# Optimization experiments

Hardware: AMD Instinct MI355X
Metric: run time of the kernel (lower is better)

Reference implementation:

```python
import jax, jax.numpy as jnp
import numpy as np

B, L, S = 128, 80, 8          # dialogues, utterances per dialogue, speakers
NODE_DIM, HIDDEN, HEADS, OUT_DIM = 768, 512, 8, 256
N = B * L


def _build_edges():
    """Replicates InterSentenceGNN.build_graph + Batch.from_data_list offsets."""
    rel = np.zeros((N, 3), np.float32)
    all_e, last = [], []
    eye3 = np.eye(3, dtype=np.float32)
    for b in range(B):
        off = b * L
        u = L - 1
        e, t = [], []
        for i in range(L):
            if i > 0:
                e += [[i - 1, i], [i, i - 1]]; t += [0, 0]   # REL_SEQ
            if i < u:
                e += [[i, u], [u, i]]; t += [1, 1]           # REL_CTX
        for s in range(S):                                   # REL_SPK, round-robin speakers
            g = list(range(s, L, S))
            for a in range(len(g)):
                for c in range(a + 1, len(g)):
                    e += [[g[a], g[c]], [g[c], g[a]]]; t += [2, 2]
        e = np.asarray(e, np.int64); t = np.asarray(t, np.int64)
        np.add.at(rel, e[:, 0] + off, eye3[t])               # out-degree per relation (pre-unique)
        all_e.append(np.unique(e, axis=0) + off)             # torch.unique(idx, dim=1)
        last.append(off + u)
    edge_index = np.concatenate(all_e, 0).T.astype(np.int32)  # [2, E], row0=src, row1=dst
    return edge_index, rel, np.asarray(last, np.int32)


def setup_inputs() -> dict:
    key = jax.random.key(0)
    ks = jax.random.split(key, 16)
    edge_index, rel_feat, last_idx = _build_edges()
    g = lambda k, shp, fan: jax.random.normal(k, shp, jnp.float32) * (1.0 / np.sqrt(fan))
    return {
        "x": jax.random.normal(ks[0], (N, NODE_DIM), jnp.float32),
        "rel_feat": jnp.asarray(rel_feat),
        "w1": g(ks[1], (3, 64), 3), "b1": jnp.zeros((64,), jnp.float32),
        "w2": g(ks[2], (64, 1), 64), "b2": jnp.zeros((1,), jnp.float32),
        "Wl1": g(ks[3], (NODE_DIM, HIDDEN), NODE_DIM), "bl1": jnp.zeros((HIDDEN,), jnp.float32),
        "Wr1": g(ks[4], (NODE_DIM, HIDDEN), NODE_DIM), "br1": jnp.zeros((HIDDEN,), jnp.float32),
        "att1": g(ks[5], (HEADS, HIDDEN // HEADS), HIDDEN // HEADS),
        "bias1": jnp.zeros((HIDDEN,), jnp.float32),
        "Wl2": g(ks[6], (HIDDEN, OUT_DIM), HIDDEN), "bl2": jnp.zeros((OUT_DIM,), jnp.float32),
        "Wr2": g(ks[7], (HIDDEN, OUT_DIM), HIDDEN), "br2": jnp.zeros((OUT_DIM,), jnp.float32),
        "att2": g(ks[8], (1, OUT_DIM), OUT_DIM),
        "bias2": jnp.zeros((OUT_DIM,), jnp.float32),
        "ln_g": jnp.ones((OUT_DIM,), jnp.float32), "ln_b": jnp.zeros((OUT_DIM,), jnp.float32),
        "edge_index": jnp.asarray(edge_index),
        "last_idx": jnp.asarray(last_idx),
    }


def _gatv2(x, Wl, bl, Wr, br, att, bias, src, dst, heads, ch, concat):
    """PyG GATv2Conv (eval mode, self-loops already in src/dst)."""
    n = x.shape[0]
    xl = (x @ Wl + bl).reshape(n, heads, ch)   # source transform (messages)
    xr = (x @ Wr + br).reshape(n, heads, ch)   # target transform
    e = jax.nn.leaky_relu(xl[src] + xr[dst], negative_slope=0.2)  # [E,H,C]
    logit = jnp.einsum("ehc,hc->eh", e, att)                      # [E,H]
    m = jax.ops.segment_max(logit, dst, num_segments=n)
    a = jnp.exp(logit - m[dst])
    denom = jax.ops.segment_sum(a, dst, num_segments=n)
    alpha = a / denom[dst]                                        # segment softmax over dst
    msg = (xl[src] * alpha[:, :, None]).reshape(-1, heads * ch)
    out = jax.ops.segment_sum(msg, dst, num_segments=n).reshape(n, heads, ch)
    out = out.reshape(n, heads * ch) if concat else out.mean(axis=1)
    return out + bias


def reference(x, rel_feat, w1, b1, w2, b2, Wl1, bl1, Wr1, br1, att1, bias1,
              Wl2, bl2, Wr2, br2, att2, bias2, ln_g, ln_b, edge_index, last_idx):
    n = x.shape[0]
    loops = jnp.arange(n, dtype=edge_index.dtype)
    src = jnp.concatenate([edge_index[0], loops])  # add_self_loops=True (PyG default)
    dst = jnp.concatenate([edge_index[1], loops])
    w = jax.nn.sigmoid(jax.nn.relu(rel_feat @ w1 + b1) @ w2 + b2)  # [N,1] node gate
    h = x * w
    h = jax.nn.elu(_gatv2(h, Wl1, bl1, Wr1, br1, att1, bias1, src, dst, HEADS, HIDDEN // HEADS, True))
    h = _gatv2(h, Wl2, bl2, Wr2, br2, att2, bias2, src, dst, 1, OUT_DIM, False)
    mu = jnp.mean(h, axis=-1, keepdims=True)
    var = jnp.mean((h - mu) ** 2, axis=-1, keepdims=True)
    h = (h - mu) * jax.lax.rsqrt(var + 1e-5) * ln_g + ln_b
    return h[last_idx]  # x[batch.ptr[1:] - 1]: last (context) node per dialogue
```

## Files before the change

kernel.cpp:

```cpp
#include <hip/hip_runtime.h>
#include <hip/hip_bf16.h>

#define NN 10240
#define LL 80
#define BB 128

typedef _Float16 half8 __attribute__((ext_vector_type(8)));
typedef _Float16 half2v __attribute__((ext_vector_type(2)));
typedef float f32x4 __attribute__((ext_vector_type(4)));

#define GLD16(gptr, lptr)                                                        \
  __builtin_amdgcn_global_load_lds(                                              \
      (const __attribute__((address_space(1))) void*)(gptr),                     \
      (__attribute__((address_space(3))) void*)(lptr), 16, 0, 0)

__device__ __forceinline__ float dot2f(half2v a, half2v b, float c) {
#if __has_builtin(__builtin_amdgcn_fdot2)
  return __builtin_amdgcn_fdot2(a, b, c, false);
#else
  return c + (float)a.x * (float)b.x + (float)a.y * (float)b.y;
#endif
}
__device__ __forceinline__ half2v u2h(unsigned int u) { half2v r; __builtin_memcpy(&r, &u, 4); return r; }
__device__ __forceinline__ unsigned int h2u(half2v h) { unsigned int u; __builtin_memcpy(&u, &h, 4); return u; }
__device__ __forceinline__ int roff(int r) { return r * 72; }

__device__ __forceinline__ float dotq4r(uint4 a, uint4 b, const half2v* atv, int qb, float acc) {
  const half2v c02 = {(_Float16)0.2f, (_Float16)0.2f};
  unsigned int aa[4] = {a.x, a.y, a.z, a.w};
  unsigned int bb[4] = {b.x, b.y, b.z, b.w};
#pragma unroll
  for (int j = 0; j < 4; ++j) {
    half2v e = u2h(aa[j]) + u2h(bb[j]);
    half2v l = __builtin_elementwise_max(e, e * c02);
    acc = dot2f(l, atv[qb + j], acc);
  }
  return acc;
}

__global__ __launch_bounds__(256) void prep_all(
    const float* __restrict__ x, const float* __restrict__ rel,
    const float* __restrict__ w1, const float* __restrict__ b1,
    const float* __restrict__ w2, const float* __restrict__ b2,
    const float* __restrict__ Wl1, const float* __restrict__ Wr1,
    const float* __restrict__ Wl2, const float* __restrict__ Wr2,
    const float* __restrict__ bl1, const float* __restrict__ br1,
    const float* __restrict__ att1,
    _Float16* __restrict__ h0, _Float16* __restrict__ Wt1,
    _Float16* __restrict__ Wt2cat,
    float* __restrict__ biasc, _Float16* __restrict__ att_h) {
  __shared__ float tile[32][33];
  int bid = blockIdx.x;
  int tid = threadIdx.x;
  if (bid < 2560) {
    int wave = tid >> 6, l = tid & 63;
    int n = bid * 4 + wave;
    float r0 = rel[n * 3 + 0], r1 = rel[n * 3 + 1], r2 = rel[n * 3 + 2];
    float v = r0 * w1[l] + r1 * w1[64 + l] + r2 * w1[128 + l] + b1[l];
    v = v > 0.f ? v : 0.f;
    v *= w2[l];
    for (int d = 32; d; d >>= 1) v += __shfl_down(v, d, 64);
    float s = __shfl(v, 0, 64);
    float g = 1.f / (1.f + __expf(-(s + b2[0])));
    const float4* xr = (const float4*)(x + (size_t)n * 768);
    _Float16* hr = h0 + (size_t)n * 768;
#pragma unroll
    for (int i = 0; i < 3; ++i) {
      int f = i * 64 + l;
      float4 xv = xr[f];
      half2v p0 = {(_Float16)(xv.x * g), (_Float16)(xv.y * g)};
      half2v p1 = {(_Float16)(xv.z * g), (_Float16)(xv.w * g)};
      uint2 ov = {h2u(p0), h2u(p1)};
      *(uint2*)&hr[f * 4] = ov;
    }
    return;
  }
  int r = bid - 2560;
  const float* W;
  _Float16* Wt;
  int K, Nc, bx, by;
  if (r < 384)      { W = Wl1; Wt = Wt1;                          K = 768; Nc = 512; bx = r % 16;       by = r / 16; }
  else if (r < 768) { W = Wr1; Wt = Wt1 + (size_t)512 * 768;      K = 768; Nc = 512; bx = (r-384) % 16; by = (r-384) / 16; }
  else if (r < 896) { W = Wl2; Wt = Wt2cat;                       K = 512; Nc = 256; bx = (r-768) % 8;  by = (r-768) / 8; }
  else if (r < 1024){ W = Wr2; Wt = Wt2cat + (size_t)256 * 512;   K = 512; Nc = 256; bx = (r-896) % 8;  by = (r-896) / 8; }
  else {
    for (int i = tid; i < 1024; i += 256) biasc[i] = (i < 512) ? bl1[i] : br1[i - 512];
    for (int i = tid; i < 512; i += 256) att_h[i] = (_Float16)att1[i];
    return;
  }
  int n0 = bx * 32, k0 = by * 32;
  int c = tid & 31, rr = tid >> 5;
#pragma unroll
  for (int p = 0; p < 4; ++p) {
    int rw = p * 8 + rr;
    tile[rw][c] = W[(size_t)(k0 + rw) * Nc + n0 + c];
  }
  __syncthreads();
#pragma unroll
  for (int p = 0; p < 4; ++p) {
    int rw = p * 8 + rr;
    Wt[(size_t)(n0 + rw) * K + k0 + c] = (_Float16)tile[c][rw];
  }
}

__global__ __launch_bounds__(512, 6) void gemm1gat1(
    const _Float16* __restrict__ h0, const _Float16* __restrict__ Wt1,
    const float* __restrict__ biasc, const _Float16* __restrict__ att_h,
    const float* __restrict__ bias1, _Float16* __restrict__ h1) {
  __shared__ __align__(16) char smem[53248];
  _Float16* Ab = (_Float16*)smem;
  _Float16* Bb = (_Float16*)(smem + 20480);
  _Float16* s_xl = (_Float16*)smem;
  _Float16* s_xr = (_Float16*)(smem + 11520);
  float* s_logit = (float*)(smem + 23040);
  signed char* s_src8 = (signed char*)(smem + 27200);
  float* s_hub = (float*)(smem + 28240);
  _Float16* s_xlT = (_Float16*)(smem + 28560);
  _Float16* s_P = (_Float16*)smem;

  int bx = blockIdx.x;
  int h = bx >> 7, b = bx & 127;
  int base = b * LL;
  int tid = threadIdx.x;
  int wave = tid >> 6, lane = tid & 63;
  int lr = lane & 15, lk = lane >> 4;

  int segA8 = ((lane & 7) ^ ((lane >> 3) & 7)) * 8;
  int r0a = wave * 16 + (lane >> 3);
  const _Float16* aP0 = h0;
  const _Float16* aP1 = h0;
  if (wave < 5) {
    aP0 = h0 + (size_t)(base + r0a) * 768 + segA8;
    aP1 = h0 + (size_t)(base + r0a + 8) * 768 + segA8;
  }
  int rb0 = r0a, rb1 = r0a + 8;
  int wr0 = (rb0 < 64) ? (h * 64 + rb0) : (512 + h * 64 + (rb0 - 64));
  int wr1 = (rb1 < 64) ? (h * 64 + rb1) : (512 + h * 64 + (rb1 - 64));
  const _Float16* bP0 = Wt1 + (size_t)wr0 * 768 + segA8;
  const _Float16* bP1 = Wt1 + (size_t)wr1 * 768 + segA8;

  f32x4 acc[5] = {};
  if (wave < 5) {
    GLD16(aP0, Ab + wave * 1024);
    GLD16(aP1, Ab + wave * 1024 + 512);
  }
  GLD16(bP0, Bb + wave * 1024);
  GLD16(bP1, Bb + wave * 1024 + 512);
  __syncthreads();
  for (int t = 0; t < 12; ++t) {
    int cur = t & 1;
    if (t < 11) {
      int k0 = (t + 1) * 64;
      int nb = cur ^ 1;
      if (wave < 5) {
        GLD16(aP0 + k0, Ab + nb * 5120 + wave * 1024);
        GLD16(aP1 + k0, Ab + nb * 5120 + wave * 1024 + 512);
      }
      GLD16(bP0 + k0, Bb + nb * 8192 + wave * 1024);
      GLD16(bP1 + k0, Bb + nb * 8192 + wave * 1024 + 512);
    }
    const _Float16* Ac = Ab + cur * 5120;
    const _Float16* Bc = Bb + cur * 8192;
    int rB = wave * 16 + lr;
#pragma unroll
    for (int s2 = 0; s2 < 2; ++s2) {
      int cx = ((s2 * 4 + lk) ^ (lr & 7)) * 8;
      half8 bf = *(const half8*)(Bc + rB * 64 + cx);
#pragma unroll
      for (int m = 0; m < 5; ++m) {
        half8 af = *(const half8*)(Ac + (m * 16 + lr) * 64 + cx);
        acc[m] = __builtin_amdgcn_mfma_f32_16x16x32_f16(af, bf, acc[m], 0, 0, 0);
      }
    }
    __syncthreads();
  }
  {
    int c = wave * 16 + lr;
    bool isxl = c < 64;
    int cc = isxl ? c : c - 64;
    float bb = biasc[(isxl ? 0 : 512) + h * 64 + cc];
    _Float16* dst = isxl ? s_xl : s_xr;
#pragma unroll
    for (int m = 0; m < 5; ++m)
#pragma unroll
      for (int rg = 0; rg < 4; ++rg) {
        int row = m * 16 + lk * 4 + rg;
        _Float16 hv = (_Float16)(acc[m][rg] + bb);
        dst[roff(row) + cc] = hv;
        if (isxl) s_xlT[cc * 88 + row] = hv;
      }
  }
  if (tid < 79) {
    int d = tid;
    signed char list[13];
    int c = 0;
    list[c++] = (signed char)d;
    if (d > 0) list[c++] = (signed char)(d - 1);
    if (d + 1 < 79) list[c++] = (signed char)(d + 1);
    list[c++] = 79;
    for (int j = d & 7; j < 80; j += 8)
      if (j != d && j != 79) list[c++] = (signed char)j;
    for (int i = c; i < 13; ++i) list[i] = -1;
#pragma unroll
    for (int i = 0; i < 13; ++i) s_src8[i * 80 + d] = list[i];
  }
  __syncthreads();

  const unsigned int* pat = (const unsigned int*)(att_h + h * 64);
  half2v atv[32];
#pragma unroll
  for (int q = 0; q < 32; ++q) atv[q] = u2h(__builtin_amdgcn_readfirstlane(pat[q]));
  if (tid < 474) {
    int d = tid / 6, io = tid % 6;
    const uint4* pxr = (const uint4*)(s_xr + roff(d));
    uint4 xrr[8];
#pragma unroll
    for (int q = 0; q < 8; ++q) xrr[q] = pxr[q];
#pragma unroll
    for (int k = 0; k < 3; ++k) {
      int i = io + 6 * k;
      if (i < 13) {
        int src = s_src8[i * 80 + d];
        if (src < 0) {
          s_logit[i * 80 + d] = -3e38f;
        } else {
          const uint4* pxl = (const uint4*)(s_xl + roff(src));
          float a2 = 0.f;
#pragma unroll
          for (int q = 0; q < 8; ++q) a2 = dotq4r(pxl[q], xrr[q], atv, q * 4, a2);
          s_logit[i * 80 + d] = a2;
        }
      }
    }
  } else {
    int j = tid - 474;
    const uint4* pxr = (const uint4*)(s_xr + roff(79));
    uint4 xrr[8];
#pragma unroll
    for (int q = 0; q < 8; ++q) xrr[q] = pxr[q];
#pragma unroll
    for (int k = 0; k < 3; ++k) {
      int s = j + 38 * k;
      if (s < 80) {
        const uint4* pxl = (const uint4*)(s_xl + roff(s));
        float a2 = 0.f;
#pragma unroll
        for (int q = 0; q < 8; ++q) a2 = dotq4r(pxl[q], xrr[q], atv, q * 4, a2);
        s_hub[s] = a2;
      }
    }
  }
  __syncthreads();

  {
    uint4 z4 = {0u, 0u, 0u, 0u};
    for (int z = tid; z < 1040; z += 512) ((uint4*)smem)[z] = z4;
  }
  float va[13], inv_d = 0.f;
  bool isd = tid < 79;
  if (isd) {
    int d = tid;
    float m = -3e38f;
#pragma unroll
    for (int i = 0; i < 13; ++i) { va[i] = s_logit[i * 80 + d]; m = fmaxf(m, va[i]); }
    float sum = 0.f;
#pragma unroll
    for (int i = 0; i < 13; ++i) { va[i] = __expf(va[i] - m); sum += va[i]; }
    inv_d = 1.f / sum;
  }
  float he0 = 0.f, he1 = 0.f, hinv = 0.f;
  if (wave == 7) {
    int l = lane;
    float v0 = s_hub[l];
    float v1 = (l < 16) ? s_hub[64 + l] : -3e38f;
    float m = fmaxf(v0, v1);
    for (int d = 32; d; d >>= 1) m = fmaxf(m, __shfl_xor(m, d, 64));
    he0 = __expf(v0 - m);
    he1 = (l < 16) ? __expf(v1 - m) : 0.f;
    float sum = he0 + he1;
    for (int d = 32; d; d >>= 1) sum += __shfl_xor(sum, d, 64);
    hinv = 1.f / sum;
  }
  __syncthreads();

  if (isd) {
    int d = tid;
#pragma unroll
    for (int i = 0; i < 13; ++i) {
      int src = s_src8[i * 80 + d];
      if (src >= 0) s_P[d * 104 + src] = (_Float16)(va[i] * inv_d);
    }
  }
  if (wave == 7) {
    int l = lane;
    s_P[79 * 104 + l] = (_Float16)(he0 * hinv);
    if (l < 16) s_P[79 * 104 + 64 + l] = (_Float16)(he1 * hinv);
  }
  __syncthreads();

  {
    int nt = (wave < 4) ? 3 : 2;
    int tb = (wave < 4) ? wave * 3 : 12 + (wave - 4) * 2;
    for (int tt = 0; tt < nt; ++tt) {
      int t = tb + tt;
      int m = t >> 2, n = t & 3;
      f32x4 a = {};
#pragma unroll
      for (int kc = 0; kc < 3; ++kc) {
        half8 af = *(const half8*)(s_P + (m * 16 + lr) * 104 + kc * 32 + lk * 8);
        half8 bf = *(const half8*)(s_xlT + (n * 16 + lr) * 88 + kc * 32 + lk * 8);
        a = __builtin_amdgcn_mfma_f32_16x16x32_f16(af, bf, a, 0, 0, 0);
      }
      int c = n * 16 + lr;
      float bb = bias1[h * 64 + c];
#pragma unroll
      for (int rg = 0; rg < 4; ++rg) {
        int d = m * 16 + lk * 4 + rg;
        float v = a[rg] + bb;
        v = v > 0.f ? v : __expf(v) - 1.f;
        h1[(size_t)(base + d) * 512 + h * 64 + c] = (_Float16)v;
      }
    }
  }
}

__global__ __launch_bounds__(256) void gemm2a(
    const _Float16* __restrict__ h1, const _Float16* __restrict__ Bt,
    const float* __restrict__ bl2, _Float16* __restrict__ xl2) {
  __shared__ __align__(16) char smem[16384];
  _Float16* Ab = (_Float16*)smem;
  _Float16* Bb = (_Float16*)(smem + 8192);
  int bx = blockIdx.x;
  int mb = bx >> 2, nb = bx & 3;
  int tid = threadIdx.x;
  int wave = tid >> 6, lane = tid & 63;
  int lr = lane & 15, lk = lane >> 4;
  int seg8 = ((lane & 3) ^ ((lane >> 3) & 3)) * 8;
  int row = tid >> 2;
  const _Float16* aP = h1 + (size_t)(mb * 64 + row) * 512 + seg8;
  const _Float16* bP = Bt + (size_t)(nb * 64 + row) * 512 + seg8;
  int xk8 = (lk ^ ((lr >> 1) & 3)) * 8;
  f32x4 acc[4] = {};
  GLD16(aP, Ab + wave * 512);
  GLD16(bP, Bb + wave * 512);
  __syncthreads();
  for (int t = 0; t < 16; ++t) {
    int cur = t & 1;
    if (t < 15) {
      int k0 = (t + 1) * 32;
      int nbuf = cur ^ 1;
      GLD16(aP + k0, Ab + nbuf * 2048 + wave * 512);
      GLD16(bP + k0, Bb + nbuf * 2048 + wave * 512);
    }
    const _Float16* Ac = Ab + cur * 2048;
    const _Float16* Bc = Bb + cur * 2048;
    half8 bf = *(const half8*)(Bc + (wave * 16 + lr) * 32 + xk8);
#pragma unroll
    for (int m = 0; m < 4; ++m) {
      half8 af = *(const half8*)(Ac + (m * 16 + lr) * 32 + xk8);
      acc[m] = __builtin_amdgcn_mfma_f32_16x16x32_f16(af, bf, acc[m], 0, 0, 0);
    }
    __syncthreads();
  }
  int col = nb * 64 + wave * 16 + lr;
  float bb = bl2[col];
#pragma unroll
  for (int m = 0; m < 4; ++m)
#pragma unroll
    for (int rg = 0; rg < 4; ++rg) {
      int r = mb * 64 + m * 16 + lk * 4 + rg;
      xl2[(size_t)r * 256 + col] = (_Float16)(acc[m][rg] + bb);
    }
}

#define PX 264
__global__ __launch_bounds__(512) void gat2ln(
    const _Float16* __restrict__ h1, const _Float16* __restrict__ xl2,
    const _Float16* __restrict__ Bt, const float* __restrict__ br2,
    const float* __restrict__ att2, const float* __restrict__ bias2,
    const float* __restrict__ ln_g, const float* __restrict__ ln_b,
    float* __restrict__ out) {
  __shared__ __align__(16) _Float16 s_x[80 * PX];
  __shared__ _Float16 s_att[256];
  __shared__ _Float16 s_xr[256];
  __shared__ float s_red[80];
  __shared__ float s_sum[4], s_sq[4];

  int b = blockIdx.x;
  int tid = threadIdx.x;
  int wave = tid >> 6, lane = tid & 63;

  if (tid < 256) s_att[tid] = (_Float16)att2[tid];
  for (int t = tid; t < 2560; t += 512) {
    int row = t >> 5, q = t & 31;
    uint4 v = *(const uint4*)(xl2 + ((size_t)(b * 80 + row)) * 256 + q * 8);
    *(uint4*)(s_x + row * PX + q * 8) = v;
  }
  {
    int c = tid >> 1, kh = tid & 1;
    const uint4* wr = (const uint4*)(Bt + (size_t)(256 + c) * 512 + kh * 256);
    const uint4* hq = (const uint4*)(h1 + (size_t)(b * 80 + 79) * 512 + kh * 256);
    float s = 0.f;
#pragma unroll 8
    for (int q = 0; q < 32; ++q) {
      uint4 ua = hq[q], uw = wr[q];
      s = dot2f(u2h(ua.x), u2h(uw.x), s);
      s = dot2f(u2h(ua.y), u2h(uw.y), s);
      s = dot2f(u2h(ua.z), u2h(uw.z), s);
      s = dot2f(u2h(ua.w), u2h(uw.w), s);
    }
    s += __shfl_xor(s, 1, 64);
    if (kh == 0) s_xr[c] = (_Float16)(s + br2[c]);
  }
  __syncthreads();
  if (tid < 160) {
    int r = tid >> 1, hf = tid & 1;
    const half2v* xa = (const half2v*)(s_x + r * PX + hf * 128);
    const half2v* xr = (const half2v*)(s_xr + hf * 128);
    const half2v* at = (const half2v*)(s_att + hf * 128);
    float lg = 0.f;
    const half2v c02 = {(_Float16)0.2f, (_Float16)0.2f};
#pragma unroll
    for (int q = 0; q < 64; ++q) {
      half2v e = xa[q] + xr[q];
      half2v l = __builtin_elementwise_max(e, e * c02);
      lg = dot2f(l, at[q], lg);
    }
    lg += __shfl_xor(lg, 1, 64);
    if (hf == 0) s_red[r] = lg;
  }
  __syncthreads();
  if (wave == 7) {
    float v0 = s_red[lane];
    float v1 = (lane < 16) ? s_red[64 + lane] : -3e38f;
    float m = fmaxf(v0, v1);
    for (int d = 32; d; d >>= 1) m = fmaxf(m, __shfl_xor(m, d, 64));
    float e0 = __expf(v0 - m);
    float e1 = (lane < 16) ? __expf(v1 - m) : 0.f;
    float sum = e0 + e1;
    for (int d = 32; d; d >>= 1) sum += __shfl_xor(sum, d, 64);
    float inv = 1.f / sum;
    s_red[lane] = e0 * inv;
    if (lane < 16) s_red[64 + lane] = e1 * inv;
  }
  __syncthreads();
  float v = 0.f;
  if (tid < 256) {
    float a = 0.f;
#pragma unroll
    for (int r = 0; r < 80; ++r) a += s_red[r] * (float)s_x[r * PX + tid];
    v = a + bias2[tid];
    float p = v;
    for (int d = 32; d; d >>= 1) p += __shfl_down(p, d, 64);
    if (lane == 0) s_sum[wave] = p;
    float q = v * v;
    for (int d = 32; d; d >>= 1) q += __shfl_down(q, d, 64);
    if (lane == 0) s_sq[wave] = q;
  }
  __syncthreads();
  if (tid < 256) {
    float mu = (s_sum[0] + s_sum[1] + s_sum[2] + s_sum[3]) * (1.f / 256.f);
    float ex2 = (s_sq[0] + s_sq[1] + s_sq[2] + s_sq[3]) * (1.f / 256.f);
    float var = ex2 - mu * mu;
    float r = rsqrtf(var + 1e-5f);
    out[b * 256 + tid] = (v - mu) * r * ln_g[tid] + ln_b[tid];
  }
}

extern "C" void kernel_launch(void* const* d_in, const int* in_sizes, int n_in,
                              void* d_out, int out_size, void* d_ws, size_t ws_size,
                              hipStream_t stream) {
  const float* x      = (const float*)d_in[0];
  const float* rel    = (const float*)d_in[1];
  const float* w1     = (const float*)d_in[2];
  const float* b1     = (const float*)d_in[3];
  const float* w2     = (const float*)d_in[4];
  const float* b2     = (const float*)d_in[5];
  const float* Wl1    = (const float*)d_in[6];
  const float* bl1    = (const float*)d_in[7];
  const float* Wr1    = (const float*)d_in[8];
  const float* br1    = (const float*)d_in[9];
  const float* att1   = (const float*)d_in[10];
  const float* bias1  = (const float*)d_in[11];
  const float* Wl2    = (const float*)d_in[12];
  const float* bl2    = (const float*)d_in[13];
  const float* Wr2    = (const float*)d_in[14];
  const float* br2    = (const float*)d_in[15];
  const float* att2   = (const float*)d_in[16];
  const float* bias2  = (const float*)d_in[17];
  const float* ln_g   = (const float*)d_in[18];
  const float* ln_b   = (const float*)d_in[19];
  float* out = (float*)d_out;

  char* p = (char*)d_ws;
  _Float16* h0     = (_Float16*)p; p += (size_t)NN * 768 * 2;
  _Float16* h1     = (_Float16*)p; p += (size_t)NN * 512 * 2;
  _Float16* Wt1    = (_Float16*)p; p += (size_t)1024 * 768 * 2;
  _Float16* Wt2cat = (_Float16*)p; p += (size_t)512 * 512 * 2;
  _Float16* att_h  = (_Float16*)p; p += 1024;
  float* biasc     = (float*)p; p += 1024 * 4;
  _Float16* xl2    = (_Float16*)p; p += (size_t)NN * 256 * 2;

  prep_all<<<2560 + 1025, 256, 0, stream>>>(x, rel, w1, b1, w2, b2, Wl1, Wr1, Wl2, Wr2,
                                            bl1, br1, att1, h0, Wt1, Wt2cat, biasc, att_h);

  gemm1gat1<<<1024, 512, 0, stream>>>(h0, Wt1, biasc, att_h, bias1, h1);

  gemm2a<<<640, 256, 0, stream>>>(h1, Wt2cat, bl2, xl2);

  gat2ln<<<BB, 512, 0, stream>>>(h1, xl2, Wt2cat, br2, att2, bias2, ln_g, ln_b, out);
}
```

Measured before the change: 179.8 us.

## Process two attention heads per block in fused GEMM1+GAT1 kernel

Each block of the fused projection plus first-layer attention kernel now computes two heads instead of one, so the grid is halved. The block loads its slab of node features once and multiplies it against both heads' weight columns, using a narrower 32-wide K step with a new swizzle. The attention and softmax stage then runs twice in sequence, once per head, over separate shared-memory buffers. This halves the global reads of the node features and drops the grid to one wave of resident blocks, at the cost of a larger shared-memory footprint (lower occupancy), twice the accumulator registers, and more serialized work per block.

```diff
diff --git a/kernel.cpp b/kernel.cpp
--- a/kernel.cpp
+++ b/kernel.cpp
@@ -107,88 +107,89 @@
     const _Float16* __restrict__ h0, const _Float16* __restrict__ Wt1,
     const float* __restrict__ biasc, const _Float16* __restrict__ att_h,
     const float* __restrict__ bias1, _Float16* __restrict__ h1) {
-  __shared__ __align__(16) char smem[53248];
+  __shared__ __align__(16) char smem[74240];
   _Float16* Ab = (_Float16*)smem;
-  _Float16* Bb = (_Float16*)(smem + 20480);
-  _Float16* s_xl = (_Float16*)smem;
-  _Float16* s_xr = (_Float16*)(smem + 11520);
-  float* s_logit = (float*)(smem + 23040);
-  signed char* s_src8 = (signed char*)(smem + 27200);
-  float* s_hub = (float*)(smem + 28240);
-  _Float16* s_xlT = (_Float16*)(smem + 28560);
+  _Float16* Bb = (_Float16*)(smem + 10240);
+  _Float16* s_xl0 = (_Float16*)smem;
+  _Float16* s_xr0 = (_Float16*)(smem + 11520);
+  _Float16* s_xl1 = (_Float16*)(smem + 23040);
+  _Float16* s_xr1 = (_Float16*)(smem + 34560);
+  float* s_logit = (float*)(smem + 46080);
+  signed char* s_src8 = (signed char*)(smem + 50240);
+  float* s_hub = (float*)(smem + 51280);
+  _Float16* s_xlT0 = (_Float16*)(smem + 51600);
+  _Float16* s_xlT1 = (_Float16*)(smem + 62864);
   _Float16* s_P = (_Float16*)smem;
 
   int bx = blockIdx.x;
-  int h = bx >> 7, b = bx & 127;
+  int hp = bx >> 7, b = bx & 127;
   int base = b * LL;
   int tid = threadIdx.x;
   int wave = tid >> 6, lane = tid & 63;
   int lr = lane & 15, lk = lane >> 4;
 
-  int segA8 = ((lane & 7) ^ ((lane >> 3) & 7)) * 8;
-  int r0a = wave * 16 + (lane >> 3);
-  const _Float16* aP0 = h0;
-  const _Float16* aP1 = h0;
+  int seg8 = ((lane & 3) ^ ((lane >> 3) & 3)) * 8;
+  const _Float16* aP = h0;
   if (wave < 5) {
-    aP0 = h0 + (size_t)(base + r0a) * 768 + segA8;
-    aP1 = h0 + (size_t)(base + r0a + 8) * 768 + segA8;
-  }
-  int rb0 = r0a, rb1 = r0a + 8;
-  int wr0 = (rb0 < 64) ? (h * 64 + rb0) : (512 + h * 64 + (rb0 - 64));
-  int wr1 = (rb1 < 64) ? (h * 64 + rb1) : (512 + h * 64 + (rb1 - 64));
-  const _Float16* bP0 = Wt1 + (size_t)wr0 * 768 + segA8;
-  const _Float16* bP1 = Wt1 + (size_t)wr1 * 768 + segA8;
-
-  f32x4 acc[5] = {};
-  if (wave < 5) {
-    GLD16(aP0, Ab + wave * 1024);
-    GLD16(aP1, Ab + wave * 1024 + 512);
-  }
+    int c = wave * 64 + lane;
+    aP = h0 + (size_t)(base + (c >> 2)) * 768 + seg8;
+  }
+  int c0 = wave * 128 + lane;
+  int r0 = c0 >> 2, r1 = (c0 + 64) >> 2;
+  int rh0 = r0 & 127, rh1 = r1 & 127;
+  int hh0 = hp * 2 + (r0 >> 7), hh1 = hp * 2 + (r1 >> 7);
+  int w0 = (rh0 < 64) ? (hh0 * 64 + rh0) : (512 + hh0 * 64 + (rh0 - 64));
+  int w1 = (rh1 < 64) ? (hh1 * 64 + rh1) : (512 + hh1 * 64 + (rh1 - 64));
+  const _Float16* bP0 = Wt1 + (size_t)w0 * 768 + seg8;
+  const _Float16* bP1 = Wt1 + (size_t)w1 * 768 + seg8;
+  int xk8 = (lk ^ ((lr >> 1) & 3)) * 8;
+
+  f32x4 acc[5][2] = {};
+  if (wave < 5) GLD16(aP, Ab + wave * 512);
   GLD16(bP0, Bb + wave * 1024);
   GLD16(bP1, Bb + wave * 1024 + 512);
   __syncthreads();
-  for (int t = 0; t < 12; ++t) {
+  for (int t = 0; t < 24; ++t) {
     int cur = t & 1;
-    if (t < 11) {
-      int k0 = (t + 1) * 64;
+    if (t < 23) {
+      int k0 = (t + 1) * 32;
       int nb = cur ^ 1;
-      if (wave < 5) {
-        GLD16(aP0 + k0, Ab + nb * 5120 + wave * 1024);
-        GLD16(aP1 + k0, Ab + nb * 5120 + wave * 1024 + 512);
-      }
+      if (wave < 5) GLD16(aP + k0, Ab + nb * 2560 + wave * 512);
       GLD16(bP0 + k0, Bb + nb * 8192 + wave * 1024);
       GLD16(bP1 + k0, Bb + nb * 8192 + wave * 1024 + 512);
     }
-    const _Float16* Ac = Ab + cur * 5120;
+    const _Float16* Ac = Ab + cur * 2560;
     const _Float16* Bc = Bb + cur * 8192;
-    int rB = wave * 16 + lr;
-#pragma unroll
-    for (int s2 = 0; s2 < 2; ++s2) {
-      int cx = ((s2 * 4 + lk) ^ (lr & 7)) * 8;
-      half8 bf = *(const half8*)(Bc + rB * 64 + cx);
-#pragma unroll
-      for (int m = 0; m < 5; ++m) {
-        half8 af = *(const half8*)(Ac + (m * 16 + lr) * 64 + cx);
-        acc[m] = __builtin_amdgcn_mfma_f32_16x16x32_f16(af, bf, acc[m], 0, 0, 0);
-      }
+    half8 bf0 = *(const half8*)(Bc + (wave * 16 + lr) * 32 + xk8);
+    half8 bf1 = *(const half8*)(Bc + ((wave + 8) * 16 + lr) * 32 + xk8);
+#pragma unroll
+    for (int m = 0; m < 5; ++m) {
+      half8 af = *(const half8*)(Ac + (m * 16 + lr) * 32 + xk8);
+      acc[m][0] = __builtin_amdgcn_mfma_f32_16x16x32_f16(af, bf0, acc[m][0], 0, 0, 0);
+      acc[m][1] = __builtin_amdgcn_mfma_f32_16x16x32_f16(af, bf1, acc[m][1], 0, 0, 0);
     }
     __syncthreads();
   }
   {
-    int c = wave * 16 + lr;
-    bool isxl = c < 64;
-    int cc = isxl ? c : c - 64;
-    float bb = biasc[(isxl ? 0 : 512) + h * 64 + cc];
-    _Float16* dst = isxl ? s_xl : s_xr;
-#pragma unroll
-    for (int m = 0; m < 5; ++m)
-#pragma unroll
-      for (int rg = 0; rg < 4; ++rg) {
-        int row = m * 16 + lk * 4 + rg;
-        _Float16 hv = (_Float16)(acc[m][rg] + bb);
-        dst[roff(row) + cc] = hv;
-        if (isxl) s_xlT[cc * 88 + row] = hv;
-      }
+    int c2 = wave * 16 + lr;
+    bool isxl = c2 < 64;
+    int cc = isxl ? c2 : c2 - 64;
+#pragma unroll
+    for (int hj = 0; hj < 2; ++hj) {
+      int h = hp * 2 + hj;
+      float bb = biasc[(isxl ? 0 : 512) + h * 64 + cc];
+      _Float16* dst = hj ? (isxl ? s_xl1 : s_xr1) : (isxl ? s_xl0 : s_xr0);
+      _Float16* xlT = hj ? s_xlT1 : s_xlT0;
+#pragma unroll
+      for (int m = 0; m < 5; ++m)
+#pragma unroll
+        for (int rg = 0; rg < 4; ++rg) {
+          int row = m * 16 + lk * 4 + rg;
+          _Float16 hv = (_Float16)(acc[m][hj][rg] + bb);
+          dst[roff(row) + cc] = hv;
+          if (isxl) xlT[cc * 88 + row] = hv;
+        }
+    }
   }
   if (tid < 79) {
     int d = tid;
@@ -206,121 +207,128 @@
   }
   __syncthreads();
 
-  const unsigned int* pat = (const unsigned int*)(att_h + h * 64);
-  half2v atv[32];
-#pragma unroll
-  for (int q = 0; q < 32; ++q) atv[q] = u2h(__builtin_amdgcn_readfirstlane(pat[q]));
-  if (tid < 474) {
-    int d = tid / 6, io = tid % 6;
-    const uint4* pxr = (const uint4*)(s_xr + roff(d));
-    uint4 xrr[8];
-#pragma unroll
-    for (int q = 0; q < 8; ++q) xrr[q] = pxr[q];
-#pragma unroll
-    for (int k = 0; k < 3; ++k) {
-      int i = io + 6 * k;
-      if (i < 13) {
-        int src = s_src8[i * 80 + d];
-        if (src < 0) {
-          s_logit[i * 80 + d] = -3e38f;
-        } else {
-          const uint4* pxl = (const uint4*)(s_xl + roff(src));
-          float a2 = 0.f;
-#pragma unroll
-          for (int q = 0; q < 8; ++q) a2 = dotq4r(pxl[q], xrr[q], atv, q * 4, a2);
-          s_logit[i * 80 + d] = a2;
+  for (int hj = 0; hj < 2; ++hj) {
+    int h = hp * 2 + hj;
+    _Float16* xlC = hj ? s_xl1 : s_xl0;
+    _Float16* xrC = hj ? s_xr1 : s_xr0;
+    _Float16* xlTC = hj ? s_xlT1 : s_xlT0;
+    const unsigned int* pat = (const unsigned int*)(att_h + h * 64);
+    half2v atv[32];
+#pragma unroll
+    for (int q = 0; q < 32; ++q) atv[q] = u2h(__builtin_amdgcn_readfirstlane(pat[q]));
+    if (tid < 474) {
+      int d = tid / 6, io = tid % 6;
+      const uint4* pxr = (const uint4*)(xrC + roff(d));
+      uint4 xrr[8];
+#pragma unroll
+      for (int q = 0; q < 8; ++q) xrr[q] = pxr[q];
+#pragma unroll
+      for (int k = 0; k < 3; ++k) {
+        int i = io + 6 * k;
+        if (i < 13) {
+          int src = s_src8[i * 80 + d];
+          if (src < 0) {
+            s_logit[i * 80 + d] = -3e38f;
+          } else {
+            const uint4* pxl = (const uint4*)(xlC + roff(src));
+            float a2 = 0.f;
+#pragma unroll
+            for (int q = 0; q < 8; ++q) a2 = dotq4r(pxl[q], xrr[q], atv, q * 4, a2);
+            s_logit[i * 80 + d] = a2;
+          }
         }
       }
-    }
-  } else {
-    int j = tid - 474;
-    const uint4* pxr = (const uint4*)(s_xr + roff(79));
-    uint4 xrr[8];
-#pragma unroll
-    for (int q = 0; q < 8; ++q) xrr[q] = pxr[q];
-#pragma unroll
-    for (int k = 0; k < 3; ++k) {
-      int s = j + 38 * k;
-      if (s < 80) {
-        const uint4* pxl = (const uint4*)(s_xl + roff(s));
-        float a2 = 0.f;
-#pragma unroll
-        for (int q = 0; q < 8; ++q) a2 = dotq4r(pxl[q], xrr[q], atv, q * 4, a2);
-        s_hub[s] = a2;
+    } else {
+      int j = tid - 474;
+      const uint4* pxr = (const uint4*)(xrC + roff(79));
+      uint4 xrr[8];
+#pragma unroll
+      for (int q = 0; q < 8; ++q) xrr[q] = pxr[q];
+#pragma unroll
+      for (int k = 0; k < 3; ++k) {
+        int s = j + 38 * k;
+        if (s < 80) {
+          const uint4* pxl = (const uint4*)(xlC + roff(s));
+          float a2 = 0.f;
+#pragma unroll
+          for (int q = 0; q < 8; ++q) a2 = dotq4r(pxl[q], xrr[q], atv, q * 4, a2);
+          s_hub[s] = a2;
+        }
       }
     }
-  }
-  __syncthreads();
-
-  {
-    uint4 z4 = {0u, 0u, 0u, 0u};
-    for (int z = tid; z < 1040; z += 512) ((uint4*)smem)[z] = z4;
-  }
-  float va[13], inv_d = 0.f;
-  bool isd = tid < 79;
-  if (isd) {
-    int d = tid;
-    float m = -3e38f;
-#pragma unroll
-    for (int i = 0; i < 13; ++i) { va[i] = s_logit[i * 80 + d]; m = fmaxf(m, va[i]); }
-    float sum = 0.f;
-#pragma unroll
-    for (int i = 0; i < 13; ++i) { va[i] = __expf(va[i] - m); sum += va[i]; }
-    inv_d = 1.f / sum;
-  }
-  float he0 = 0.f, he1 = 0.f, hinv = 0.f;
-  if (wave == 7) {
-    int l = lane;
-    float v0 = s_hub[l];
-    float v1 = (l < 16) ? s_hub[64 + l] : -3e38f;
-    float m = fmaxf(v0, v1);
-    for (int d = 32; d; d >>= 1) m = fmaxf(m, __shfl_xor(m, d, 64));
-    he0 = __expf(v0 - m);
-    he1 = (l < 16) ? __expf(v1 - m) : 0.f;
-    float sum = he0 + he1;
-    for (int d = 32; d; d >>= 1) sum += __shfl_xor(sum, d, 64);
-    hinv = 1.f / sum;
-  }
-  __syncthreads();
-
-  if (isd) {
-    int d = tid;
-#pragma unroll
-    for (int i = 0; i < 13; ++i) {
-      int src = s_src8[i * 80 + d];
-      if (src >= 0) s_P[d * 104 + src] = (_Float16)(va[i] * inv_d);
-    }
-  }
-  if (wave == 7) {
-    int l = lane;
-    s_P[79 * 104 + l] = (_Float16)(he0 * hinv);
-    if (l < 16) s_P[79 * 104 + 64 + l] = (_Float16)(he1 * hinv);
-  }
-  __syncthreads();
-
-  {
-    int nt = (wave < 4) ? 3 : 2;
-    int tb = (wave < 4) ? wave * 3 : 12 + (wave - 4) * 2;
-    for (int tt = 0; tt < nt; ++tt) {
-      int t = tb + tt;
-      int m = t >> 2, n = t & 3;
-      f32x4 a = {};
-#pragma unroll
-      for (int kc = 0; kc < 3; ++kc) {
-        half8 af = *(const half8*)(s_P + (m * 16 + lr) * 104 + kc * 32 + lk * 8);
-        half8 bf = *(const half8*)(s_xlT + (n * 16 + lr) * 88 + kc * 32 + lk * 8);
-        a = __builtin_amdgcn_mfma_f32_16x16x32_f16(af, bf, a, 0, 0, 0);
+    __syncthreads();
+
+    {
+      uint4 z4 = {0u, 0u, 0u, 0u};
+      for (int z = tid; z < 1040; z += 512) ((uint4*)smem)[z] = z4;
+    }
+    float va[13], inv_d = 0.f;
+    bool isd = tid < 79;
+    if (isd) {
+      int d = tid;
+      float m = -3e38f;
+#pragma unroll
+      for (int i = 0; i < 13; ++i) { va[i] = s_logit[i * 80 + d]; m = fmaxf(m, va[i]); }
+      float sum = 0.f;
+#pragma unroll
+      for (int i = 0; i < 13; ++i) { va[i] = __expf(va[i] - m); sum += va[i]; }
+      inv_d = 1.f / sum;
+    }
+    float he0 = 0.f, he1 = 0.f, hinv = 0.f;
+    if (wave == 7) {
+      int l = lane;
+      float v0 = s_hub[l];
+      float v1 = (l < 16) ? s_hub[64 + l] : -3e38f;
+      float m = fmaxf(v0, v1);
+      for (int d = 32; d; d >>= 1) m = fmaxf(m, __shfl_xor(m, d, 64));
+      he0 = __expf(v0 - m);
+      he1 = (l < 16) ? __expf(v1 - m) : 0.f;
+      float sum = he0 + he1;
+      for (int d = 32; d; d >>= 1) sum += __shfl_xor(sum, d, 64);
+      hinv = 1.f / sum;
+    }
+    __syncthreads();
+
+    if (isd) {
+      int d = tid;
+#pragma unroll
+      for (int i = 0; i < 13; ++i) {
+        int src = s_src8[i * 80 + d];
+        if (src >= 0) s_P[d * 104 + src] = (_Float16)(va[i] * inv_d);
       }
-      int c = n * 16 + lr;
-      float bb = bias1[h * 64 + c];
-#pragma unroll
-      for (int rg = 0; rg < 4; ++rg) {
-        int d = m * 16 + lk * 4 + rg;
-        float v = a[rg] + bb;
-        v = v > 0.f ? v : __expf(v) - 1.f;
-        h1[(size_t)(base + d) * 512 + h * 64 + c] = (_Float16)v;
+    }
+    if (wave == 7) {
+      int l = lane;
+      s_P[79 * 104 + l] = (_Float16)(he0 * hinv);
+      if (l < 16) s_P[79 * 104 + 64 + l] = (_Float16)(he1 * hinv);
+    }
+    __syncthreads();
+
+    {
+      int nt = (wave < 4) ? 3 : 2;
+      int tb = (wave < 4) ? wave * 3 : 12 + (wave - 4) * 2;
+      for (int tt = 0; tt < nt; ++tt) {
+        int t = tb + tt;
+        int m = t >> 2, n = t & 3;
+        f32x4 a = {};
+#pragma unroll
+        for (int kc = 0; kc < 3; ++kc) {
+          half8 af = *(const half8*)(s_P + (m * 16 + lr) * 104 + kc * 32 + lk * 8);
+          half8 bf = *(const half8*)(xlTC + (n * 16 + lr) * 88 + kc * 32 + lk * 8);
+          a = __builtin_amdgcn_mfma_f32_16x16x32_f16(af, bf, a, 0, 0, 0);
+        }
+        int c = n * 16 + lr;
+        float bb = bias1[h * 64 + c];
+#pragma unroll
+        for (int rg = 0; rg < 4; ++rg) {
+          int d = m * 16 + lk * 4 + rg;
+          float v = a[rg] + bb;
+          v = v > 0.f ? v : __expf(v) - 1.f;
+          h1[(size_t)(base + d) * 512 + h * 64 + c] = (_Float16)v;
+        }
       }
     }
+    __syncthreads();
   }
 }
 
@@ -504,7 +512,7 @@
   prep_all<<<2560 + 1025, 256, 0, stream>>>(x, rel, w1, b1, w2, b2, Wl1, Wr1, Wl2, Wr2,
                                             bl1, br1, att1, h0, Wt1, Wt2cat, biasc, att_h);
 
-  gemm1gat1<<<1024, 512, 0, stream>>>(h0, Wt1, biasc, att_h, bias1, h1);
+  gemm1gat1<<<512, 512, 0, stream>>>(h0, Wt1, biasc, att_h, bias1, h1);
 
   gemm2a<<<640, 256, 0, stream>>>(h1, Wt2cat, bl2, xl2);
 
```

After: 182.0 us. No clear change (+1.3%).

## Halve GEMM1 K-tile to 32 to cut LDS and raise occupancy

Applied to the files above, without the earlier changes.

The fused GEMM+GAT layer-1 kernel now stages 32-wide K tiles instead of 64-wide ones. Each lane issues one global-to-LDS load per operand per step, with a new XOR swizzle, and the loop runs 24 steps instead of 12. This shrinks the shared-memory footprint so launch bounds can request 8 blocks per SM instead of 6, trading more barriers and loop iterations for higher occupancy. It also adds explicit zeroing of the padding region of the transposed xl buffer.

```diff
diff --git a/kernel.cpp b/kernel.cpp
--- a/kernel.cpp
+++ b/kernel.cpp
@@ -103,13 +103,13 @@
   }
 }
 
-__global__ __launch_bounds__(512, 6) void gemm1gat1(
+__global__ __launch_bounds__(512, 8) void gemm1gat1(
     const _Float16* __restrict__ h0, const _Float16* __restrict__ Wt1,
     const float* __restrict__ biasc, const _Float16* __restrict__ att_h,
     const float* __restrict__ bias1, _Float16* __restrict__ h1) {
-  __shared__ __align__(16) char smem[53248];
+  __shared__ __align__(16) char smem[39936];
   _Float16* Ab = (_Float16*)smem;
-  _Float16* Bb = (_Float16*)(smem + 20480);
+  _Float16* Bb = (_Float16*)(smem + 10240);
   _Float16* s_xl = (_Float16*)smem;
   _Float16* s_xr = (_Float16*)(smem + 11520);
   float* s_logit = (float*)(smem + 23040);
@@ -125,52 +125,44 @@
   int wave = tid >> 6, lane = tid & 63;
   int lr = lane & 15, lk = lane >> 4;
 
-  int segA8 = ((lane & 7) ^ ((lane >> 3) & 7)) * 8;
-  int r0a = wave * 16 + (lane >> 3);
-  const _Float16* aP0 = h0;
-  const _Float16* aP1 = h0;
+  {
+    int z = tid;
+    int rr2 = z >> 3, kk = z & 7;
+    if (z < 512) s_xlT[rr2 * 88 + 80 + kk] = (_Float16)0.f;
+    if (z < 8) s_xlT[64 * 88 + z] = (_Float16)0.f;
+  }
+
+  int seg8 = ((lane & 3) ^ ((lane >> 3) & 3)) * 8;
+  const _Float16* aP = h0;
   if (wave < 5) {
-    aP0 = h0 + (size_t)(base + r0a) * 768 + segA8;
-    aP1 = h0 + (size_t)(base + r0a + 8) * 768 + segA8;
-  }
-  int rb0 = r0a, rb1 = r0a + 8;
-  int wr0 = (rb0 < 64) ? (h * 64 + rb0) : (512 + h * 64 + (rb0 - 64));
-  int wr1 = (rb1 < 64) ? (h * 64 + rb1) : (512 + h * 64 + (rb1 - 64));
-  const _Float16* bP0 = Wt1 + (size_t)wr0 * 768 + segA8;
-  const _Float16* bP1 = Wt1 + (size_t)wr1 * 768 + segA8;
+    int c = wave * 64 + lane;
+    aP = h0 + (size_t)(base + (c >> 2)) * 768 + seg8;
+  }
+  int cB = wave * 64 + lane;
+  int brow = cB >> 2;
+  int wrow = (brow < 64) ? (h * 64 + brow) : (512 + h * 64 + (brow - 64));
+  const _Float16* bP = Wt1 + (size_t)wrow * 768 + seg8;
+  int xk8 = (lk ^ ((lr >> 1) & 3)) * 8;
 
   f32x4 acc[5] = {};
-  if (wave < 5) {
-    GLD16(aP0, Ab + wave * 1024);
-    GLD16(aP1, Ab + wave * 1024 + 512);
-  }
-  GLD16(bP0, Bb + wave * 1024);
-  GLD16(bP1, Bb + wave * 1024 + 512);
-  __syncthreads();
-  for (int t = 0; t < 12; ++t) {
+  if (wave < 5) GLD16(aP, Ab + wave * 512);
+  GLD16(bP, Bb + wave * 512);
+  __syncthreads();
+  for (int t = 0; t < 24; ++t) {
     int cur = t & 1;
-    if (t < 11) {
-      int k0 = (t + 1) * 64;
+    if (t < 23) {
+      int k0 = (t + 1) * 32;
       int nb = cur ^ 1;
-      if (wave < 5) {
-        GLD16(aP0 + k0, Ab + nb * 5120 + wave * 1024);
-        GLD16(aP1 + k0, Ab + nb * 5120 + wave * 1024 + 512);
-      }
-      GLD16(bP0 + k0, Bb + nb * 8192 + wave * 1024);
-      GLD16(bP1 + k0, Bb + nb * 8192 + wave * 1024 + 512);
-    }
-    const _Float16* Ac = Ab + cur * 5120;
-    const _Float16* Bc = Bb + cur * 8192;
-    int rB = wave * 16 + lr;
-#pragma unroll
-    for (int s2 = 0; s2 < 2; ++s2) {
-      int cx = ((s2 * 4 + lk) ^ (lr & 7)) * 8;
-      half8 bf = *(const half8*)(Bc + rB * 64 + cx);
-#pragma unroll
-      for (int m = 0; m < 5; ++m) {
-        half8 af = *(const half8*)(Ac + (m * 16 + lr) * 64 + cx);
-        acc[m] = __builtin_amdgcn_mfma_f32_16x16x32_f16(af, bf, acc[m], 0, 0, 0);
-      }
+      if (wave < 5) GLD16(aP + k0, Ab + nb * 2560 + wave * 512);
+      GLD16(bP + k0, Bb + nb * 4096 + wave * 512);
+    }
+    const _Float16* Ac = Ab + cur * 2560;
+    const _Float16* Bc = Bb + cur * 4096;
+    half8 bf = *(const half8*)(Bc + (wave * 16 + lr) * 32 + xk8);
+#pragma unroll
+    for (int m = 0; m < 5; ++m) {
+      half8 af = *(const half8*)(Ac + (m * 16 + lr) * 32 + xk8);
+      acc[m] = __builtin_amdgcn_mfma_f32_16x16x32_f16(af, bf, acc[m], 0, 0, 0);
     }
     __syncthreads();
   }
```

After: 181.2 us. About the same (+0.8%).
